# Optimization experiments

Hardware: AMD Instinct MI355X
Metric: run time of the kernel (lower is better)

Reference implementation:

```python
import jax, jax.numpy as jnp
import numpy as np

B, D, U = 8192, 512, 512


def setup_inputs() -> dict:
    key = jax.random.key(0)
    ks = jax.random.split(key, 5)
    return {
        "inputs": jax.random.normal(ks[0], (B, D), dtype=jnp.float32),
        "h_tm1": jax.random.normal(ks[1], (B, U), dtype=jnp.float32),
        "c_tm1": jax.random.normal(ks[2], (B, U), dtype=jnp.float32),
        "kernel": jax.random.normal(ks[3], (D, 4 * U), dtype=jnp.float32) * (1.0 / np.sqrt(D)),
        "recurrent_kernel": jax.random.normal(ks[4], (U, 4 * U), dtype=jnp.float32) * (1.0 / np.sqrt(U)),
        "bias": jnp.zeros((4 * U,), dtype=jnp.float32),
    }


def reference(inputs, h_tm1, c_tm1, kernel, recurrent_kernel, bias):
    # z: [B, 4U] = x @ W + h @ R + b
    z = inputs @ kernel + h_tm1 @ recurrent_kernel + bias
    z0, z1, z2, z3 = jnp.split(z, 4, axis=1)
    i = jax.nn.sigmoid(z0)
    f = jax.nn.sigmoid(z1)
    g = jnp.tanh(z2)
    o = jax.nn.sigmoid(z3)
    c = f * c_tm1 + i * g
    h = o * jnp.tanh(c)
    return (h, h, c)
```

## Files before the change

kernel.cpp:

```cpp
#include <hip/hip_runtime.h>
#include <hip/hip_bf16.h>
#include <cstdint>
#include <cstddef>

#define BB 8192
#define UU 512
#define KPACK 1024
#define NPACK 2048

using frag16 = __attribute__((ext_vector_type(8))) short;
using f32x4  = __attribute__((ext_vector_type(4))) float;

__device__ inline float fast_sigmoid(float x) { return 1.0f / (1.0f + __expf(-x)); }
__device__ inline float fast_tanh(float x) {
  x = fminf(fmaxf(x, -15.f), 15.f);
  float e = __expf(-2.0f * x);
  return (1.0f - e) / (1.0f + e);
}

__device__ inline unsigned cvt2(float lo, float hi) {
  __hip_bfloat162 b = __float22bfloat162_rn(float2{lo, hi});
  union { __hip_bfloat162 b; unsigned u; } v; v.b = b;
  return v.u;
}

__global__ __launch_bounds__(256) void pack_kernel(const float* __restrict__ x,
                                                   const float* __restrict__ h,
                                                   const float* __restrict__ W,
                                                   const float* __restrict__ R,
                                                   short* __restrict__ Xp,
                                                   short* __restrict__ Bt) {
  if (blockIdx.x < 4096) {
    int idx = blockIdx.x * 256 + threadIdx.x;
    int row = idx >> 7;
    int k8  = (idx & 127) << 3;
    const float* src = (k8 < 512) ? (x + (size_t)row * 512 + k8)
                                  : (h + (size_t)row * 512 + (k8 - 512));
    float4 a = *(const float4*)(src);
    float4 b = *(const float4*)(src + 4);
    uint4 o;
    o.x = cvt2(a.x, a.y);
    o.y = cvt2(a.z, a.w);
    o.z = cvt2(b.x, b.y);
    o.w = cvt2(b.z, b.w);
    *(uint4*)(Xp + ((size_t)idx << 3)) = o;
  } else {
    __shared__ float tile[64][65];
    int b2 = blockIdx.x - 4096;
    int nb = (b2 & 31) * 64;
    int kb = (b2 >> 5) * 64;
    int t  = threadIdx.x;
#pragma unroll
    for (int rep = 0; rep < 16; ++rep) {
      int kr = rep * 4 + (t >> 6);
      int c  = t & 63;
      int kg = kb + kr;
      const float* s = (kg < 512) ? (W + (size_t)kg * 2048) : (R + (size_t)(kg - 512) * 2048);
      tile[c][kr] = s[nb + c];
    }
    __syncthreads();
#pragma unroll
    for (int rep = 0; rep < 4; ++rep) {
      int nn = rep * 16 + (t >> 4);
      int k4 = (t & 15) << 2;
      uint2 o;
      o.x = cvt2(tile[nn][k4 + 0], tile[nn][k4 + 1]);
      o.y = cvt2(tile[nn][k4 + 2], tile[nn][k4 + 3]);
      *(uint2*)(Bt + (size_t)(nb + nn) * 1024 + kb + k4) = o;
    }
  }
}

__global__ __launch_bounds__(512, 2) void lstm_mfma_kernel(
    const short* __restrict__ A,
    const short* __restrict__ Bt,
    const float* __restrict__ bias,
    const float* __restrict__ cprev,
    float* __restrict__ out)
{
  __shared__ short lds[3 * 24576];

  const int tid  = threadIdx.x;
  const int lane = tid & 63;
  const int wave = tid >> 6;
  const int wm   = wave & 3;
  const int wn   = wave >> 2;
  const int bm   = blockIdx.x;
  const int bn   = blockIdx.y;

  const int r8  = lane >> 3;
  const int kg  = lane & 7;
  const int kgx = kg ^ r8;

  const short* ga[4];
  int la_off[4];
#pragma unroll
  for (int t = 0; t < 4; ++t) {
    int rowl = wave * 32 + t * 8 + r8;
    ga[t] = A + (size_t)(bm * 256 + rowl) * 1024 + kgx * 8;
    la_off[t] = (wave * 32 + t * 8) * 64;
  }
  const short* gb[2];
  int lb_off[2];
#pragma unroll
  for (int t = 0; t < 2; ++t) {
    int rowl = wave * 16 + t * 8 + r8;
    int u    = bn * 32 + ((rowl >> 6) << 4) + (rowl & 15);
    int gate = (rowl >> 4) & 3;
    gb[t] = Bt + (size_t)(gate * 512 + u) * 1024 + kgx * 8;
    lb_off[t] = (wave * 16 + t * 8) * 64;
  }

  const int q   = lane >> 4;
  const int c16 = lane & 15;
  const int mx  = c16 & 7;

  auto STAGE = [&](int T, int bi) {
    const int k0 = T * 64;
    short* base = &lds[bi * 24576];
#pragma unroll
    for (int t = 0; t < 4; ++t)
      __builtin_amdgcn_global_load_lds(
          (const __attribute__((address_space(1))) void*)(ga[t] + k0),
          (__attribute__((address_space(3))) void*)(base + la_off[t]), 16, 0, 0);
#pragma unroll
    for (int t = 0; t < 2; ++t)
      __builtin_amdgcn_global_load_lds(
          (const __attribute__((address_space(1))) void*)(gb[t] + k0),
          (__attribute__((address_space(3))) void*)(base + 16384 + lb_off[t]), 16, 0, 0);
  };

  f32x4 acc[4][4];
#pragma unroll
  for (int i = 0; i < 4; ++i)
#pragma unroll
    for (int j = 0; j < 4; ++j)
      acc[i][j] = f32x4{0.f, 0.f, 0.f, 0.f};

  STAGE(0, 0);
  STAGE(1, 1);

  int rb = 0;
  for (int T = 0; T < 16; ++T) {
    if (T < 15) asm volatile("s_waitcnt vmcnt(6)" ::: "memory");
    else        asm volatile("s_waitcnt vmcnt(0)" ::: "memory");
    __builtin_amdgcn_s_barrier();
    if (T + 2 < 16) {
      int wb = rb + 2; if (wb >= 3) wb -= 3;
      STAGE(T + 2, wb);
    }
    const short* la = &lds[rb * 24576];
    const short* lb = la + 16384;
    __builtin_amdgcn_s_setprio(1);
#pragma unroll
    for (int ks = 0; ks < 2; ++ks) {
      const int ch8 = ((((ks << 2) + q) ^ mx) << 3);
      frag16 af[4], bfv[4];
#pragma unroll
      for (int i = 0; i < 4; ++i)
        af[i] = *(const frag16*)(la + (wm * 64 + i * 16 + c16) * 64 + ch8);
#pragma unroll
      for (int j = 0; j < 4; ++j)
        bfv[j] = *(const frag16*)(lb + (wn * 64 + j * 16 + c16) * 64 + ch8);
#pragma unroll
      for (int i = 0; i < 4; ++i)
#pragma unroll
        for (int j = 0; j < 4; ++j)
          acc[i][j] = __builtin_amdgcn_mfma_f32_16x16x32_bf16(af[i], bfv[j], acc[i][j], 0, 0, 0);
    }
    __builtin_amdgcn_s_setprio(0);
    rb = (rb == 2) ? 0 : rb + 1;
  }

  const int u = bn * 32 + wn * 16 + c16;
  const float b0 = bias[u];
  const float b1 = bias[512 + u];
  const float b2 = bias[1024 + u];
  const float b3 = bias[1536 + u];
  float* outh0 = out;
  float* outh1 = out + (size_t)BB * UU;
  float* outc  = out + (size_t)2 * BB * UU;

#pragma unroll
  for (int i = 0; i < 4; ++i) {
    int row0 = bm * 256 + wm * 64 + i * 16 + q * 4;
#pragma unroll
    for (int r = 0; r < 4; ++r) {
      size_t off = (size_t)(row0 + r) * UU + u;
      float z0 = acc[i][0][r] + b0;
      float z1 = acc[i][1][r] + b1;
      float z2 = acc[i][2][r] + b2;
      float z3 = acc[i][3][r] + b3;
      float ig = fast_sigmoid(z0);
      float fg = fast_sigmoid(z1);
      float gg = fast_tanh(z2);
      float og = fast_sigmoid(z3);
      float cp = cprev[off];
      float cc = fg * cp + ig * gg;
      float hh = og * fast_tanh(cc);
      outh0[off] = hh;
      outh1[off] = hh;
      outc[off]  = cc;
    }
  }
}

extern "C" void kernel_launch(void* const* d_in, const int* in_sizes, int n_in,
                              void* d_out, int out_size, void* d_ws, size_t ws_size,
                              hipStream_t stream) {
  const float* x  = (const float*)d_in[0];
  const float* h  = (const float*)d_in[1];
  const float* c  = (const float*)d_in[2];
  const float* W  = (const float*)d_in[3];
  const float* R  = (const float*)d_in[4];
  const float* b  = (const float*)d_in[5];
  float* out = (float*)d_out;

  short* Xp = (short*)d_ws;
  short* Bt = Xp + (size_t)BB * KPACK;

  pack_kernel<<<4608, 256, 0, stream>>>(x, h, W, R, Xp, Bt);
  lstm_mfma_kernel<<<dim3(32, 16), 512, 0, stream>>>(Xp, Bt, b, c, out);
}
```

Before: 154.5 us.

## Enlarge GEMM tile to 256x256 with double buffering and quadrant-phased MFMA schedule

Doubles the N tile per block from 128 to 256 columns, so each wave owns a 128x64 accumulator region and the grid shrinks to 32x8 blocks. The A operand is reused across twice as many columns, which cuts global and LDS traffic per FLOP. The triple-buffered LDS ring becomes a double buffer with full vmcnt(0) waits. Each K step now runs four barrier-separated quadrant phases that interleave fragment loads with MFMA bursts. The cost is more accumulator registers (128 floats per lane), which may spill or cut occupancy under launch_bounds(512,2), plus more barriers and less prefetch depth.

Result: no change. 153.1 us (-0.9%).

```diff
diff --git a/kernel.cpp b/kernel.cpp
--- a/kernel.cpp
+++ b/kernel.cpp
@@ -78,13 +78,13 @@
     const float* __restrict__ cprev,
     float* __restrict__ out)
 {
-  __shared__ short lds[3 * 24576];
+  __shared__ short lds[2 * 32768];
 
   const int tid  = threadIdx.x;
   const int lane = tid & 63;
   const int wave = tid >> 6;
-  const int wm   = wave & 3;
-  const int wn   = wave >> 2;
+  const int wm   = wave >> 2;
+  const int wn   = wave & 3;
   const int bm   = blockIdx.x;
   const int bn   = blockIdx.y;
 
@@ -94,21 +94,18 @@
 
   const short* ga[4];
   int la_off[4];
-#pragma unroll
-  for (int t = 0; t < 4; ++t) {
-    int rowl = wave * 32 + t * 8 + r8;
-    ga[t] = A + (size_t)(bm * 256 + rowl) * 1024 + kgx * 8;
-    la_off[t] = (wave * 32 + t * 8) * 64;
-  }
-  const short* gb[2];
-  int lb_off[2];
-#pragma unroll
-  for (int t = 0; t < 2; ++t) {
-    int rowl = wave * 16 + t * 8 + r8;
-    int u    = bn * 32 + ((rowl >> 6) << 4) + (rowl & 15);
-    int gate = (rowl >> 4) & 3;
-    gb[t] = Bt + (size_t)(gate * 512 + u) * 1024 + kgx * 8;
-    lb_off[t] = (wave * 16 + t * 8) * 64;
+  const short* gb[4];
+  int lb_off[4];
+#pragma unroll
+  for (int li = 0; li < 4; ++li) {
+    int rowa = li * 64 + wave * 8 + r8;
+    ga[li] = A + (size_t)(bm * 256 + rowa) * 1024 + kgx * 8;
+    la_off[li] = (li * 64 + wave * 8) * 64;
+    int n = li * 64 + wave * 8 + r8;
+    int u    = bn * 64 + ((n >> 6) << 4) + (n & 15);
+    int gate = (n >> 4) & 3;
+    gb[li] = Bt + (size_t)(gate * 512 + u) * 1024 + kgx * 8;
+    lb_off[li] = 16384 + (li * 64 + wave * 8) * 64;
   }
 
   const int q   = lane >> 4;
@@ -117,62 +114,114 @@
 
   auto STAGE = [&](int T, int bi) {
     const int k0 = T * 64;
-    short* base = &lds[bi * 24576];
-#pragma unroll
-    for (int t = 0; t < 4; ++t)
+    short* base = &lds[bi * 32768];
+#pragma unroll
+    for (int li = 0; li < 4; ++li)
       __builtin_amdgcn_global_load_lds(
-          (const __attribute__((address_space(1))) void*)(ga[t] + k0),
-          (__attribute__((address_space(3))) void*)(base + la_off[t]), 16, 0, 0);
-#pragma unroll
-    for (int t = 0; t < 2; ++t)
+          (const __attribute__((address_space(1))) void*)(ga[li] + k0),
+          (__attribute__((address_space(3))) void*)(base + la_off[li]), 16, 0, 0);
+#pragma unroll
+    for (int li = 0; li < 4; ++li)
       __builtin_amdgcn_global_load_lds(
-          (const __attribute__((address_space(1))) void*)(gb[t] + k0),
-          (__attribute__((address_space(3))) void*)(base + 16384 + lb_off[t]), 16, 0, 0);
+          (const __attribute__((address_space(1))) void*)(gb[li] + k0),
+          (__attribute__((address_space(3))) void*)(base + lb_off[li]), 16, 0, 0);
   };
 
-  f32x4 acc[4][4];
-#pragma unroll
-  for (int i = 0; i < 4; ++i)
+  f32x4 acc[8][4];
+#pragma unroll
+  for (int i = 0; i < 8; ++i)
 #pragma unroll
     for (int j = 0; j < 4; ++j)
       acc[i][j] = f32x4{0.f, 0.f, 0.f, 0.f};
 
   STAGE(0, 0);
-  STAGE(1, 1);
-
-  int rb = 0;
-  for (int T = 0; T < 16; ++T) {
-    if (T < 15) asm volatile("s_waitcnt vmcnt(6)" ::: "memory");
-    else        asm volatile("s_waitcnt vmcnt(0)" ::: "memory");
-    __builtin_amdgcn_s_barrier();
-    if (T + 2 < 16) {
-      int wb = rb + 2; if (wb >= 3) wb -= 3;
-      STAGE(T + 2, wb);
-    }
-    const short* la = &lds[rb * 24576];
+
+  auto CH = [&](int ks) { return (((ks << 2) + q) ^ mx) << 3; };
+
+  for (int t = 0; t < 16; ++t) {
+    const int rb = t & 1;
+    asm volatile("s_waitcnt vmcnt(0)" ::: "memory");
+    __builtin_amdgcn_s_barrier();
+    const short* la = &lds[rb * 32768];
     const short* lb = la + 16384;
-    __builtin_amdgcn_s_setprio(1);
-#pragma unroll
-    for (int ks = 0; ks < 2; ++ks) {
-      const int ch8 = ((((ks << 2) + q) ^ mx) << 3);
-      frag16 af[4], bfv[4];
-#pragma unroll
-      for (int i = 0; i < 4; ++i)
-        af[i] = *(const frag16*)(la + (wm * 64 + i * 16 + c16) * 64 + ch8);
-#pragma unroll
-      for (int j = 0; j < 4; ++j)
-        bfv[j] = *(const frag16*)(lb + (wn * 64 + j * 16 + c16) * 64 + ch8);
-#pragma unroll
-      for (int i = 0; i < 4; ++i)
-#pragma unroll
-        for (int j = 0; j < 4; ++j)
-          acc[i][j] = __builtin_amdgcn_mfma_f32_16x16x32_bf16(af[i], bfv[j], acc[i][j], 0, 0, 0);
-    }
-    __builtin_amdgcn_s_setprio(0);
-    rb = (rb == 2) ? 0 : rb + 1;
-  }
-
-  const int u = bn * 32 + wn * 16 + c16;
+
+    frag16 af[4][2], bq[2][2];
+
+#pragma unroll
+    for (int i = 0; i < 4; ++i)
+#pragma unroll
+      for (int ks = 0; ks < 2; ++ks)
+        af[i][ks] = *(const frag16*)(la + (wm * 128 + i * 16 + c16) * 64 + CH(ks));
+#pragma unroll
+    for (int j = 0; j < 2; ++j)
+#pragma unroll
+      for (int ks = 0; ks < 2; ++ks)
+        bq[j][ks] = *(const frag16*)(lb + (wn * 64 + j * 16 + c16) * 64 + CH(ks));
+    if (t + 1 < 16) STAGE(t + 1, rb ^ 1);
+    __builtin_amdgcn_s_barrier();
+    __builtin_amdgcn_s_setprio(1);
+#pragma unroll
+    for (int i = 0; i < 4; ++i)
+#pragma unroll
+      for (int j = 0; j < 2; ++j)
+#pragma unroll
+        for (int ks = 0; ks < 2; ++ks)
+          acc[i][j] = __builtin_amdgcn_mfma_f32_16x16x32_bf16(af[i][ks], bq[j][ks], acc[i][j], 0, 0, 0);
+    __builtin_amdgcn_s_setprio(0);
+    __builtin_amdgcn_s_barrier();
+
+#pragma unroll
+    for (int j = 0; j < 2; ++j)
+#pragma unroll
+      for (int ks = 0; ks < 2; ++ks)
+        bq[j][ks] = *(const frag16*)(lb + (wn * 64 + (2 + j) * 16 + c16) * 64 + CH(ks));
+    __builtin_amdgcn_s_barrier();
+    __builtin_amdgcn_s_setprio(1);
+#pragma unroll
+    for (int i = 0; i < 4; ++i)
+#pragma unroll
+      for (int j = 0; j < 2; ++j)
+#pragma unroll
+        for (int ks = 0; ks < 2; ++ks)
+          acc[i][2 + j] = __builtin_amdgcn_mfma_f32_16x16x32_bf16(af[i][ks], bq[j][ks], acc[i][2 + j], 0, 0, 0);
+    __builtin_amdgcn_s_setprio(0);
+    __builtin_amdgcn_s_barrier();
+
+#pragma unroll
+    for (int i = 0; i < 4; ++i)
+#pragma unroll
+      for (int ks = 0; ks < 2; ++ks)
+        af[i][ks] = *(const frag16*)(la + (wm * 128 + (4 + i) * 16 + c16) * 64 + CH(ks));
+    __builtin_amdgcn_s_barrier();
+    __builtin_amdgcn_s_setprio(1);
+#pragma unroll
+    for (int i = 0; i < 4; ++i)
+#pragma unroll
+      for (int j = 0; j < 2; ++j)
+#pragma unroll
+        for (int ks = 0; ks < 2; ++ks)
+          acc[4 + i][2 + j] = __builtin_amdgcn_mfma_f32_16x16x32_bf16(af[i][ks], bq[j][ks], acc[4 + i][2 + j], 0, 0, 0);
+    __builtin_amdgcn_s_setprio(0);
+    __builtin_amdgcn_s_barrier();
+
+#pragma unroll
+    for (int j = 0; j < 2; ++j)
+#pragma unroll
+      for (int ks = 0; ks < 2; ++ks)
+        bq[j][ks] = *(const frag16*)(lb + (wn * 64 + j * 16 + c16) * 64 + CH(ks));
+    __builtin_amdgcn_s_barrier();
+    __builtin_amdgcn_s_setprio(1);
+#pragma unroll
+    for (int i = 0; i < 4; ++i)
+#pragma unroll
+      for (int j = 0; j < 2; ++j)
+#pragma unroll
+        for (int ks = 0; ks < 2; ++ks)
+          acc[4 + i][j] = __builtin_amdgcn_mfma_f32_16x16x32_bf16(af[i][ks], bq[j][ks], acc[4 + i][j], 0, 0, 0);
+    __builtin_amdgcn_s_setprio(0);
+  }
+
+  const int u = bn * 64 + wn * 16 + c16;
   const float b0 = bias[u];
   const float b1 = bias[512 + u];
   const float b2 = bias[1024 + u];
@@ -182,8 +231,8 @@
   float* outc  = out + (size_t)2 * BB * UU;
 
 #pragma unroll
-  for (int i = 0; i < 4; ++i) {
-    int row0 = bm * 256 + wm * 64 + i * 16 + q * 4;
+  for (int i = 0; i < 8; ++i) {
+    int row0 = bm * 256 + wm * 128 + i * 16 + q * 4;
 #pragma unroll
     for (int r = 0; r < 4; ++r) {
       size_t off = (size_t)(row0 + r) * UU + u;
@@ -220,5 +269,5 @@
   short* Bt = Xp + (size_t)BB * KPACK;
 
   pack_kernel<<<4608, 256, 0, stream>>>(x, h, W, R, Xp, Bt);
-  lstm_mfma_kernel<<<dim3(32, 16), 512, 0, stream>>>(Xp, Bt, b, c, out);
-}
+  lstm_mfma_kernel<<<dim3(32, 8), 512, 0, stream>>>(Xp, Bt, b, c, out);
+}
```
